# Kernel tuning notes

Measured on AMD Instinct MI355X. Metric: run time of the kernel, lower is better.

The kernel has to match this reference:

```python
import jax, jax.numpy as jnp
import numpy as np

B, T, TEMP_IN, STAT_IN = 8, 512, 32, 16
TEMP_H, STAT_H, ATTN_H, N_LAYERS, N_CLS = 64, 32, 32, 2, 2
BN_INV = float(1.0 / np.sqrt(1.0 + 1e-5))  # eval-mode BN, running_mean=0, running_var=1


def _bn(x, g, b):
    return x * (g * BN_INV) + b


def _lrelu(x):
    return jax.nn.leaky_relu(x, 0.01)


def _mlp_layer(x, W, b, g, beta):
    return _lrelu(_bn(x @ W + b, g, beta))


def setup_inputs() -> dict:
    key = jax.random.key(0)
    ks = jax.random.split(key, 32)
    lengths = jax.random.randint(ks[0], (B,), T // 2, T + 1)
    mask_q = jnp.arange(T)[None, :] < lengths[:, None]          # [B,T]
    masks = mask_q[:, :, None]                                   # [B,T,1] bool
    x_temp = jax.random.normal(ks[1], (B, T, TEMP_IN), jnp.float32) * mask_q[..., None]
    x_stat = jax.random.normal(ks[2], (B, STAT_IN), jnp.float32)
    t = jnp.sort(jax.random.uniform(ks[3], (B, T), jnp.float32) * 100.0, axis=-1)
    p = lambda k, sh, s=0.1: jax.random.normal(k, sh, jnp.float32) * s
    inp = dict(x_temp=x_temp, x_stat=x_stat, t=t, masks=masks, lengths=lengths)
    # attn_mlp: Linear(1,H)+BN+LeakyReLU, Linear(H,1)
    inp['aw0'] = p(ks[4], (1, ATTN_H), 0.5); inp['ab0'] = p(ks[5], (ATTN_H,))
    inp['ag'] = 1.0 + p(ks[6], (ATTN_H,)); inp['abeta'] = p(ks[7], (ATTN_H,))
    inp['aw1'] = p(ks[8], (ATTN_H, 1), 0.2); inp['ab1'] = p(ks[9], (1,))
    # top non_linear_temp / non_linear_stat
    inp['tw'] = p(ks[10], (TEMP_IN, TEMP_H)); inp['tb'] = p(ks[11], (TEMP_H,))
    inp['tg'] = 1.0 + p(ks[12], (TEMP_H,)); inp['tbeta'] = p(ks[13], (TEMP_H,))
    inp['sw'] = p(ks[14], (STAT_IN, STAT_H)); inp['sb'] = p(ks[15], (STAT_H,))
    inp['sg'] = 1.0 + p(ks[16], (STAT_H,)); inp['sbeta'] = p(ks[17], (STAT_H,))
    # stacked SimtaPlusLayer params [L,...]
    inp['lw_t'] = p(ks[18], (N_LAYERS, TEMP_H + STAT_H, TEMP_H))
    inp['lb_t'] = p(ks[19], (N_LAYERS, TEMP_H))
    inp['lg_t'] = 1.0 + p(ks[20], (N_LAYERS, TEMP_H)); inp['lbeta_t'] = p(ks[21], (N_LAYERS, TEMP_H))
    inp['lw_s'] = p(ks[22], (N_LAYERS, STAT_H, STAT_H))
    inp['lb_s'] = p(ks[23], (N_LAYERS, STAT_H))
    inp['lg_s'] = 1.0 + p(ks[24], (N_LAYERS, STAT_H)); inp['lbeta_s'] = p(ks[25], (N_LAYERS, STAT_H))
    inp['cw'] = p(ks[26], (TEMP_H + STAT_H, N_CLS)); inp['cb'] = p(ks[27], (N_CLS,))
    return inp


def _forward(x_temp, x_stat, t, aw0, ab0, ag, abeta, aw1, ab1, tw, tb, tg, tbeta,
             sw, sb, sg, sbeta, lw_t, lb_t, lg_t, lbeta_t, lw_s, lb_s, lg_s, lbeta_s,
             cw, cb, mask_q):
    # dt[b,i,j] = (t[b,j]-t[b,i]) / (max dt + eps)
    dt = t[:, None, :] - t[:, :, None]
    dt = dt / (dt.max() + 1e-8)
    # pairwise-MLP temporal attention: [B,T,T,H] intermediate (memory-bound)
    h = _lrelu(_bn(dt[..., None] * aw0[0] + ab0, ag, abeta))
    a = (h @ aw1)[..., 0] + ab1[0]                                # [B,T,T]
    temp_attn = jax.nn.softmax(jnp.where(mask_q[:, None, :], a, -9e8), axis=-1)

    x_t = _mlp_layer(x_temp, tw, tb, tg, tbeta)                   # [B,T,Ct]
    x_s = _mlp_layer(x_stat, sw, sb, sg, sbeta)                   # [B,Cs]

    for l in range(lw_t.shape[0]):
        xs_rep = jnp.broadcast_to(x_s[:, None, :], (x_t.shape[0], x_t.shape[1], x_s.shape[-1]))
        x = _mlp_layer(jnp.concatenate([x_t, xs_rep], axis=-1), lw_t[l], lb_t[l], lg_t[l], lbeta_t[l])
        x = x * mask_q[..., None]                                 # pad_packed zeros invalid rows
        d = jnp.asarray(x.shape[-1], x.dtype)
        qk = jnp.einsum('bic,bjc->bij', x, x) / jnp.sqrt(d)
        self_attn = jax.nn.softmax(qk, axis=-1)                   # torch softmaxes over all keys (pads give qk=0)
        attn = (self_attn + temp_attn) * mask_q[:, None, :]       # masked_fill(~mask, 0) on key columns
        x_s = _mlp_layer(x_s, lw_s[l], lb_s[l], lg_s[l], lbeta_s[l])
        x_t = (attn @ x) * mask_q[..., None]

    xs_rep = jnp.broadcast_to(x_s[:, None, :], (x_t.shape[0], x_t.shape[1], x_s.shape[-1]))
    output = jnp.concatenate([x_t, xs_rep], axis=-1) @ cw + cb    # [B,T,C]
    output = output * mask_q[..., None]
    # per-segment argmax over (logit1 - logit0), gather that row
    diff = jnp.where(mask_q, output[..., 1] - output[..., 0], -1e30)
    idx = jnp.argmax(diff, axis=1)                                # [B]
    output_max = output[jnp.arange(output.shape[0]), idx]         # [B,C]
    return output, output_max


def reference(x_temp, x_stat, t, masks, lengths, aw0, ab0, ag, abeta, aw1, ab1,
              tw, tb, tg, tbeta, sw, sb, sg, sbeta,
              lw_t, lb_t, lg_t, lbeta_t, lw_s, lb_s, lg_s, lbeta_s, cw, cb):
    mask_q = jnp.any(masks, axis=-1)                              # [B,T]
    return _forward(x_temp, x_stat, t, aw0, ab0, ag, abeta, aw1, ab1, tw, tb, tg, tbeta,
                    sw, sb, sg, sbeta, lw_t, lb_t, lg_t, lbeta_t, lw_s, lb_s, lg_s, lbeta_s,
                    cw, cb, mask_q)
```

## Files before the change

### kernel.cpp

```cpp
#include <hip/hip_runtime.h>

#define B 8
#define T 512
#define TEMP_IN 32
#define STAT_IN 16
#define TEMP_H 64
#define STAT_H 32
#define ATTN_H 32
#define N_CLS 2
#define BN_INV 0.99999500003749969f
#define R 8

struct KP {
    const float *x_temp, *x_stat, *t;
    const int* lengths;
    const float *aw0, *ab0, *ag, *abeta, *aw1, *ab1;
    const float *tw, *tb, *tg, *tbeta;
    const float *sw, *sb, *sg, *sbeta;
    const float *lw_t, *lb_t, *lg_t, *lbeta_t;
    const float *lw_s, *lb_s, *lg_s, *lbeta_s;
    const float *cw, *cb;
    float *XL, *XL2;
    unsigned long long* cand;
    unsigned *f1, *f2;
    unsigned *arr;
    float *out, *outmax;
};

__device__ __forceinline__ float lrelu(float x) {
    return fmaxf(x, 0.01f * x);
}
__device__ __forceinline__ float wave_max(float x) {
    #pragma unroll
    for (int o = 32; o > 0; o >>= 1) x = fmaxf(x, __shfl_xor(x, o));
    return x;
}
__device__ __forceinline__ float wave_sum(float x) {
    #pragma unroll
    for (int o = 32; o > 0; o >>= 1) x += __shfl_xor(x, o);
    return x;
}
__device__ __forceinline__ unsigned ordf(float f) {
    unsigned u = __float_as_uint(f);
    return (u & 0x80000000u) ? ~u : (u | 0x80000000u);
}

__device__ __forceinline__ void stg_llc(float* p, float v) {
    __hip_atomic_store(p, v, __ATOMIC_RELAXED, __HIP_MEMORY_SCOPE_AGENT);
}
__device__ __forceinline__ float ldg_llc(const float* p) {
    return __hip_atomic_load(p, __ATOMIC_RELAXED, __HIP_MEMORY_SCOPE_AGENT);
}
__device__ __forceinline__ void drain_vm() {
    asm volatile("s_waitcnt vmcnt(0)" ::: "memory");
}
__device__ __forceinline__ void fence_acq_wg() {
    __builtin_amdgcn_fence(__ATOMIC_ACQUIRE, "workgroup");
}

struct Shm {
    float att[R][T];
    float part[4][R][TEMP_H];
    float xi[R][TEMP_H];
    float x1[R][TEMP_H];
    float t_s[T];
    float s_w[3 * ATTN_H + 1];
    float xs[3][STAT_H];
    float xr[4][TEMP_IN];
    float h0s[4][TEMP_H + STAT_H];
    float o_rc[R][2];
    int lastf;
};

__device__ __forceinline__ void publish(unsigned* f) {
    drain_vm();
    __syncthreads();
    if (threadIdx.x == 0)
        __hip_atomic_store(f, 1u, __ATOMIC_RELAXED, __HIP_MEMORY_SCOPE_AGENT);
}
__device__ __forceinline__ void wait_batch(const unsigned* fbase, int tid) {
    if (tid < 64) {
        const unsigned* p = fbase + tid * 16;
        while (__hip_atomic_load(p, __ATOMIC_RELAXED, __HIP_MEMORY_SCOPE_AGENT) == 0u)
            __builtin_amdgcn_s_sleep(4);
    }
    __syncthreads();
    fence_acq_wg();
}

__device__ __forceinline__ void front(const KP& P, Shm& S, int b, int i0, int len,
                                      int lane, int wave) {
    #pragma unroll
    for (int p = 0; p < 2; ++p) {
        int r = p * 4 + wave;
        int i = i0 + r;
        int row = b * T + i;
        if (lane < TEMP_IN) S.xr[wave][lane] = P.x_temp[row * TEMP_IN + lane];
        __syncthreads();
        float acc = P.tb[lane];
        #pragma unroll
        for (int k = 0; k < TEMP_IN; ++k) acc += S.xr[wave][k] * P.tw[k * TEMP_H + lane];
        acc = acc * (P.tg[lane] * BN_INV) + P.tbeta[lane];
        S.h0s[wave][lane] = lrelu(acc);
        if (lane < STAT_H) S.h0s[wave][TEMP_H + lane] = S.xs[0][lane];
        __syncthreads();
        float a2 = P.lb_t[lane];
        #pragma unroll
        for (int k = 0; k < TEMP_H + STAT_H; ++k) a2 += S.h0s[wave][k] * P.lw_t[k * TEMP_H + lane];
        a2 = a2 * (P.lg_t[lane] * BN_INV) + P.lbeta_t[lane];
        a2 = lrelu(a2);
        stg_llc(&P.XL[(size_t)row * TEMP_H + lane], (i < len) ? a2 : 0.f);
        __syncthreads();
    }
}

__device__ __forceinline__ void temp_compute(Shm& S, float tmpv[2][8], float inv_dt,
                                             int i0, int len, int lane, int wave) {
    float ab1v = S.s_w[3 * ATTN_H];
    #pragma unroll
    for (int rr = 0; rr < 2; ++rr) {
        int r = wave + rr * 4;
        float ti = S.t_s[i0 + r];
        float a[8], dtq[8];
        #pragma unroll
        for (int q = 0; q < 8; ++q) {
            dtq[q] = (S.t_s[lane + q * 64] - ti) * inv_dt;
            a[q] = ab1v;
        }
        #pragma unroll 4
        for (int k = 0; k < ATTN_H; ++k) {
            float Wk = S.s_w[k];
            float Ck = S.s_w[ATTN_H + k];
            float w1k = S.s_w[2 * ATTN_H + k];
            #pragma unroll
            for (int q = 0; q < 8; ++q) {
                float h = dtq[q] * Wk + Ck;
                h = fmaxf(h, 0.01f * h);
                a[q] += h * w1k;
            }
        }
        float m2 = -1e30f;
        #pragma unroll
        for (int q = 0; q < 8; ++q) {
            int j = lane + q * 64;
            a[q] = (j < len) ? a[q] : -9e8f;
            m2 = fmaxf(m2, a[q]);
        }
        m2 = wave_max(m2);
        float s2 = 0.f;
        #pragma unroll
        for (int q = 0; q < 8; ++q) { a[q] = __expf(a[q] - m2); s2 += a[q]; }
        s2 = wave_sum(s2);
        float inv2 = 1.0f / s2;
        #pragma unroll
        for (int q = 0; q < 8; ++q) tmpv[rr][q] = a[q] * inv2;
    }
}

template <int EPI, bool LOAD_XI>
__device__ __forceinline__ void attn_core(const KP& P, Shm& S, const float* src,
                                          const float tmpv[2][8],
                                          int b, int i0, int len, int tid, int lane, int wave,
                                          int tile) {
    if (LOAD_XI) {
        for (int idx = tid; idx < R * TEMP_H; idx += 256)
            S.xi[idx >> 6][idx & 63] = src[((size_t)(b * T + i0 + (idx >> 6))) * TEMP_H + (idx & 63)];
    }
    __syncthreads();
    for (int j = tid; j < T; j += 256) {
        const float4* xj4 = reinterpret_cast<const float4*>(&src[((size_t)(b * T + j)) * TEMP_H]);
        float acc[R];
        #pragma unroll
        for (int r = 0; r < R; ++r) acc[r] = 0.f;
        #pragma unroll
        for (int c4 = 0; c4 < TEMP_H / 4; ++c4) {
            float4 xv = xj4[c4];
            #pragma unroll
            for (int r = 0; r < R; ++r) {
                float4 xi4 = *reinterpret_cast<const float4*>(&S.xi[r][c4 * 4]);
                acc[r] += xi4.x * xv.x + xi4.y * xv.y + xi4.z * xv.z + xi4.w * xv.w;
            }
        }
        #pragma unroll
        for (int r = 0; r < R; ++r) S.att[r][j] = acc[r] * 0.125f;
    }
    __syncthreads();
    #pragma unroll
    for (int rr = 0; rr < 2; ++rr) {
        int r = wave + rr * 4;
        float v[8];
        float m = -1e30f;
        #pragma unroll
        for (int q = 0; q < 8; ++q) { v[q] = S.att[r][lane + q * 64]; m = fmaxf(m, v[q]); }
        m = wave_max(m);
        float s = 0.f;
        #pragma unroll
        for (int q = 0; q < 8; ++q) { v[q] = __expf(v[q] - m); s += v[q]; }
        s = wave_sum(s);
        float invs = 1.0f / s;
        #pragma unroll
        for (int q = 0; q < 8; ++q) {
            int j = lane + q * 64;
            S.att[r][j] = (j < len) ? (v[q] * invs + tmpv[rr][q]) : 0.f;
        }
    }
    __syncthreads();
    float acc2[R];
    #pragma unroll
    for (int r = 0; r < R; ++r) acc2[r] = 0.f;
    {
        const float* srow = src + (size_t)b * T * TEMP_H + lane;
        int j0 = wave * 128;
        for (int g = 0; g < 32; ++g) {
            int j = j0 + g * 4;
            float xv0 = srow[(size_t)(j + 0) * TEMP_H];
            float xv1 = srow[(size_t)(j + 1) * TEMP_H];
            float xv2 = srow[(size_t)(j + 2) * TEMP_H];
            float xv3 = srow[(size_t)(j + 3) * TEMP_H];
            #pragma unroll
            for (int r = 0; r < R; ++r) {
                float4 a4 = *reinterpret_cast<const float4*>(&S.att[r][j]);
                acc2[r] += a4.x * xv0 + a4.y * xv1 + a4.z * xv2 + a4.w * xv3;
            }
        }
    }
    #pragma unroll
    for (int r = 0; r < R; ++r) S.part[wave][r][lane] = acc2[r];
    __syncthreads();
    for (int idx = tid; idx < R * TEMP_H; idx += 256) {
        int r = idx >> 6, cc = idx & 63;
        float sum = S.part[0][r][cc] + S.part[1][r][cc] + S.part[2][r][cc] + S.part[3][r][cc];
        S.x1[r][cc] = ((i0 + r) < len) ? sum : 0.f;
    }
    __syncthreads();

    if (EPI == 0) {
        const float* lw1    = P.lw_t + (TEMP_H + STAT_H) * TEMP_H;
        const float* lb1    = P.lb_t + TEMP_H;
        const float* lg1    = P.lg_t + TEMP_H;
        const float* lbeta1 = P.lbeta_t + TEMP_H;
        #pragma unroll
        for (int rr = 0; rr < 2; ++rr) {
            int r = wave * 2 + rr;
            int i = i0 + r;
            float acc = lb1[lane];
            #pragma unroll
            for (int k = 0; k < TEMP_H; ++k) acc += S.x1[r][k] * lw1[k * TEMP_H + lane];
            #pragma unroll
            for (int k = 0; k < STAT_H; ++k) acc += S.xs[1][k] * lw1[(TEMP_H + k) * TEMP_H + lane];
            acc = acc * (lg1[lane] * BN_INV) + lbeta1[lane];
            acc = lrelu(acc);
            float vout = (i < len) ? acc : 0.f;
            stg_llc(&P.XL2[((size_t)(b * T + i)) * TEMP_H + lane], vout);
            S.xi[r][lane] = vout;
        }
    } else {
        if (tid < R * N_CLS) {
            int r = tid >> 1, cls = tid & 1;
            int i = i0 + r;
            float o = P.cb[cls];
            #pragma unroll
            for (int k = 0; k < TEMP_H; ++k) o += S.x1[r][k] * P.cw[k * N_CLS + cls];
            #pragma unroll
            for (int k = 0; k < STAT_H; ++k) o += S.xs[2][k] * P.cw[(TEMP_H + k) * N_CLS + cls];
            if (i >= len) o = 0.f;
            stg_llc(&P.out[((size_t)(b * T + i)) * N_CLS + cls], o);
            S.o_rc[r][cls] = o;
        }
        __syncthreads();
        if (tid == 0) {
            float best = -3e30f; int bi = i0;
            for (int r = 0; r < R; ++r) {
                int i = i0 + r;
                float diff = (i < len) ? (S.o_rc[r][1] - S.o_rc[r][0]) : -1e30f;
                if (diff > best) { best = diff; bi = i; }
            }
            unsigned long long pack =
                ((unsigned long long)ordf(best) << 32) | (unsigned)(~(unsigned)bi);
            __hip_atomic_store(&P.cand[(b * 64 + tile) * 8], pack,
                               __ATOMIC_RELAXED, __HIP_MEMORY_SCOPE_AGENT);
            drain_vm();
            unsigned old = __hip_atomic_fetch_add(&P.arr[b * 16], 1u,
                                                  __ATOMIC_RELAXED, __HIP_MEMORY_SCOPE_AGENT);
            S.lastf = (old == 63u) ? 1 : 0;
        }
        __syncthreads();
        if (S.lastf) {
            fence_acq_wg();
            if (tid < 64) {
                unsigned long long c = __hip_atomic_load(&P.cand[(b * 64 + tid) * 8],
                                                         __ATOMIC_RELAXED, __HIP_MEMORY_SCOPE_AGENT);
                #pragma unroll
                for (int o = 32; o > 0; o >>= 1) {
                    unsigned long long oc = __shfl_xor(c, o);
                    c = (oc > c) ? oc : c;
                }
                if (tid == 0) {
                    int idx = (int)(~(unsigned)(c & 0xffffffffu));
                    float o0 = ldg_llc(&P.out[((size_t)(b * T + idx)) * N_CLS + 0]);
                    float o1 = ldg_llc(&P.out[((size_t)(b * T + idx)) * N_CLS + 1]);
                    stg_llc(&P.outmax[b * 2 + 0], o0);
                    stg_llc(&P.outmax[b * 2 + 1], o1);
                }
            }
        }
    }
}

template <int PHASE>
__global__ void __launch_bounds__(256, 2) k_run(KP P) {
    __shared__ Shm S;
    int tid = threadIdx.x, lane = tid & 63, wave = tid >> 6;
    int blk = blockIdx.x;
    int b = blk & 7, tile = blk >> 3, i0 = tile * R;
    int len = P.lengths[b];
    float tmpv[2][8];

    if (tid < STAT_H) {
        float acc = P.sb[tid];
        #pragma unroll
        for (int k = 0; k < STAT_IN; ++k) acc += P.x_stat[b * STAT_IN + k] * P.sw[k * STAT_H + tid];
        acc = acc * (P.sg[tid] * BN_INV) + P.sbeta[tid];
        S.xs[0][tid] = lrelu(acc);
    }
    __syncthreads();

    if (PHASE == 0 || PHASE == 3) front(P, S, b, i0, len, lane, wave);
    if (PHASE == 3) publish(&P.f1[(b * 64 + tile) * 16]);

    if (PHASE != 0) {
        if (tid < ATTN_H) {
            float g = P.ag[tid] * BN_INV;
            S.s_w[tid]              = P.aw0[tid] * g;
            S.s_w[ATTN_H + tid]     = P.ab0[tid] * g + P.abeta[tid];
            S.s_w[2 * ATTN_H + tid] = P.aw1[tid];
        }
        if (tid == 0) S.s_w[3 * ATTN_H] = P.ab1[0];
        S.t_s[tid] = P.t[b * T + tid];
        S.t_s[tid + 256] = P.t[b * T + tid + 256];
        float d = P.t[(lane & 7) * T + (T - 1)] - P.t[(lane & 7) * T];
        d = wave_max(d);
        float inv_dt = 1.0f / (d + 1e-8f);
        __syncthreads();
        if (tid < STAT_H) {
            float a2 = P.lb_s[tid];
            #pragma unroll
            for (int k = 0; k < STAT_H; ++k) a2 += S.xs[0][k] * P.lw_s[k * STAT_H + tid];
            a2 = a2 * (P.lg_s[tid] * BN_INV) + P.lbeta_s[tid];
            S.xs[1][tid] = lrelu(a2);
        }
        __syncthreads();
        if (tid < STAT_H) {
            float a2 = P.lb_s[STAT_H + tid];
            #pragma unroll
            for (int k = 0; k < STAT_H; ++k) a2 += S.xs[1][k] * P.lw_s[(STAT_H + k) * STAT_H + tid];
            a2 = a2 * (P.lg_s[STAT_H + tid] * BN_INV) + P.lbeta_s[STAT_H + tid];
            S.xs[2][tid] = lrelu(a2);
        }
        __syncthreads();
        temp_compute(S, tmpv, inv_dt, i0, len, lane, wave);
        __syncthreads();
    }

    if (PHASE == 3) wait_batch(P.f1 + b * 64 * 16, tid);
    if (PHASE == 1 || PHASE == 3)
        attn_core<0, true>(P, S, P.XL, tmpv, b, i0, len, tid, lane, wave, tile);
    if (PHASE == 3) {
        publish(&P.f2[(b * 64 + tile) * 16]);
        wait_batch(P.f2 + b * 64 * 16, tid);
        attn_core<1, false>(P, S, P.XL2, tmpv, b, i0, len, tid, lane, wave, tile);
    } else if (PHASE == 2) {
        attn_core<1, true>(P, S, P.XL2, tmpv, b, i0, len, tid, lane, wave, tile);
    }
}

extern "C" void kernel_launch(void* const* d_in, const int* in_sizes, int n_in,
                              void* d_out, int out_size, void* d_ws, size_t ws_size,
                              hipStream_t stream) {
    KP p;
    p.x_temp  = (const float*)d_in[0];
    p.x_stat  = (const float*)d_in[1];
    p.t       = (const float*)d_in[2];
    p.lengths = (const int*)d_in[4];
    p.aw0 = (const float*)d_in[5];
    p.ab0 = (const float*)d_in[6];
    p.ag  = (const float*)d_in[7];
    p.abeta = (const float*)d_in[8];
    p.aw1 = (const float*)d_in[9];
    p.ab1 = (const float*)d_in[10];
    p.tw  = (const float*)d_in[11];
    p.tb  = (const float*)d_in[12];
    p.tg  = (const float*)d_in[13];
    p.tbeta = (const float*)d_in[14];
    p.sw  = (const float*)d_in[15];
    p.sb  = (const float*)d_in[16];
    p.sg  = (const float*)d_in[17];
    p.sbeta = (const float*)d_in[18];
    p.lw_t = (const float*)d_in[19];
    p.lb_t = (const float*)d_in[20];
    p.lg_t = (const float*)d_in[21];
    p.lbeta_t = (const float*)d_in[22];
    p.lw_s = (const float*)d_in[23];
    p.lb_s = (const float*)d_in[24];
    p.lg_s = (const float*)d_in[25];
    p.lbeta_s = (const float*)d_in[26];
    p.cw = (const float*)d_in[27];
    p.cb = (const float*)d_in[28];

    float* ws = (float*)d_ws;
    p.XL  = ws;
    p.XL2 = ws + (size_t)B * T * TEMP_H;
    p.cand = (unsigned long long*)(ws + 2 * (size_t)B * T * TEMP_H);
    p.f1  = (unsigned*)(p.cand + B * 64 * 8);
    p.f2  = p.f1 + B * 64 * 16;
    p.arr = p.f2 + B * 64 * 16;
    p.out = (float*)d_out;
    p.outmax = p.out + (size_t)B * T * N_CLS;

    size_t flagbytes = (size_t)B * 64 * 8 * 8 + 2 * (size_t)B * 64 * 16 * 4 + (size_t)B * 16 * 4;
    hipMemsetAsync(p.cand, 0, flagbytes, stream);

    void* args[] = { (void*)&p };
    hipError_t err = hipLaunchCooperativeKernel((const void*)k_run<3>, dim3(B * (T / R)),
                                                dim3(256), args, 0, stream);
    if (err != hipSuccess) {
        (void)hipGetLastError();
        k_run<0><<<B * (T / R), 256, 0, stream>>>(p);
        k_run<1><<<B * (T / R), 256, 0, stream>>>(p);
        k_run<2><<<B * (T / R), 256, 0, stream>>>(p);
    }
}
```

Before: 103.4 us.

## Merge two row tiles into 512-thread blocks, halving grid and sync flags

Each block now runs 512 threads split into two 256-thread sides, each handling 8 query rows, so the grid shrinks from 512 to 256 blocks covering 16 rows apiece. Each batch now waits on 32 per-block flags instead of 64, which cuts grid-barrier polling, and the shared per-batch setup (time vector, stat MLP) is done once for 16 rows. Front-stage scratch now shares shared memory with the partial-sum buffer through a union. The cost is larger blocks with more shared memory and possibly lower occupancy per CU, and the grid may now fill fewer CUs.

```diff
diff --git a/kernel.cpp b/kernel.cpp
--- a/kernel.cpp
+++ b/kernel.cpp
@@ -9,7 +9,8 @@
 #define ATTN_H 32
 #define N_CLS 2
 #define BN_INV 0.99999500003749969f
-#define R 8
+#define NBLK 256
+#define NT2  32
 
 struct KP {
     const float *x_temp, *x_stat, *t;
@@ -44,7 +45,6 @@
     unsigned u = __float_as_uint(f);
     return (u & 0x80000000u) ? ~u : (u | 0x80000000u);
 }
-
 __device__ __forceinline__ void stg_llc(float* p, float v) {
     __hip_atomic_store(p, v, __ATOMIC_RELAXED, __HIP_MEMORY_SCOPE_AGENT);
 }
@@ -59,16 +59,17 @@
 }
 
 struct Shm {
-    float att[R][T];
-    float part[4][R][TEMP_H];
-    float xi[R][TEMP_H];
-    float x1[R][TEMP_H];
+    float att[2][8][T];
+    union {
+        float part[2][4][8][TEMP_H];
+        struct { float xr[8][TEMP_IN]; float h0s[8][TEMP_H + STAT_H]; } fr;
+    } u;
+    float xi[2][8][TEMP_H];
+    float x1[2][8][TEMP_H];
     float t_s[T];
     float s_w[3 * ATTN_H + 1];
     float xs[3][STAT_H];
-    float xr[4][TEMP_IN];
-    float h0s[4][TEMP_H + STAT_H];
-    float o_rc[R][2];
+    float o_rc[16][2];
     int lastf;
 };
 
@@ -79,7 +80,7 @@
         __hip_atomic_store(f, 1u, __ATOMIC_RELAXED, __HIP_MEMORY_SCOPE_AGENT);
 }
 __device__ __forceinline__ void wait_batch(const unsigned* fbase, int tid) {
-    if (tid < 64) {
+    if (tid < NT2) {
         const unsigned* p = fbase + tid * 16;
         while (__hip_atomic_load(p, __ATOMIC_RELAXED, __HIP_MEMORY_SCOPE_AGENT) == 0u)
             __builtin_amdgcn_s_sleep(4);
@@ -88,25 +89,25 @@
     fence_acq_wg();
 }
 
-__device__ __forceinline__ void front(const KP& P, Shm& S, int b, int i0, int len,
+__device__ __forceinline__ void front(const KP& P, Shm& S, int b, int i0b, int len,
                                       int lane, int wave) {
     #pragma unroll
     for (int p = 0; p < 2; ++p) {
-        int r = p * 4 + wave;
-        int i = i0 + r;
+        int r = p * 8 + wave;
+        int i = i0b + r;
         int row = b * T + i;
-        if (lane < TEMP_IN) S.xr[wave][lane] = P.x_temp[row * TEMP_IN + lane];
+        if (lane < TEMP_IN) S.u.fr.xr[wave][lane] = P.x_temp[row * TEMP_IN + lane];
         __syncthreads();
         float acc = P.tb[lane];
         #pragma unroll
-        for (int k = 0; k < TEMP_IN; ++k) acc += S.xr[wave][k] * P.tw[k * TEMP_H + lane];
+        for (int k = 0; k < TEMP_IN; ++k) acc += S.u.fr.xr[wave][k] * P.tw[k * TEMP_H + lane];
         acc = acc * (P.tg[lane] * BN_INV) + P.tbeta[lane];
-        S.h0s[wave][lane] = lrelu(acc);
-        if (lane < STAT_H) S.h0s[wave][TEMP_H + lane] = S.xs[0][lane];
+        S.u.fr.h0s[wave][lane] = lrelu(acc);
+        if (lane < STAT_H) S.u.fr.h0s[wave][TEMP_H + lane] = S.xs[0][lane];
         __syncthreads();
         float a2 = P.lb_t[lane];
         #pragma unroll
-        for (int k = 0; k < TEMP_H + STAT_H; ++k) a2 += S.h0s[wave][k] * P.lw_t[k * TEMP_H + lane];
+        for (int k = 0; k < TEMP_H + STAT_H; ++k) a2 += S.u.fr.h0s[wave][k] * P.lw_t[k * TEMP_H + lane];
         a2 = a2 * (P.lg_t[lane] * BN_INV) + P.lbeta_t[lane];
         a2 = lrelu(a2);
         stg_llc(&P.XL[(size_t)row * TEMP_H + lane], (i < len) ? a2 : 0.f);
@@ -115,12 +116,12 @@
 }
 
 __device__ __forceinline__ void temp_compute(Shm& S, float tmpv[2][8], float inv_dt,
-                                             int i0, int len, int lane, int wave) {
+                                             int i0s, int len, int lane, int swave) {
     float ab1v = S.s_w[3 * ATTN_H];
     #pragma unroll
     for (int rr = 0; rr < 2; ++rr) {
-        int r = wave + rr * 4;
-        float ti = S.t_s[i0 + r];
+        int r = swave + rr * 4;
+        float ti = S.t_s[i0s + r];
         float a[8], dtq[8];
         #pragma unroll
         for (int q = 0; q < 8; ++q) {
@@ -160,38 +161,41 @@
 template <int EPI, bool LOAD_XI>
 __device__ __forceinline__ void attn_core(const KP& P, Shm& S, const float* src,
                                           const float tmpv[2][8],
-                                          int b, int i0, int len, int tid, int lane, int wave,
-                                          int tile) {
+                                          int b, int i0b, int len,
+                                          int tid, int lane, int side, int stid, int swave,
+                                          int blk_id) {
+    int i0s = i0b + side * 8;
     if (LOAD_XI) {
-        for (int idx = tid; idx < R * TEMP_H; idx += 256)
-            S.xi[idx >> 6][idx & 63] = src[((size_t)(b * T + i0 + (idx >> 6))) * TEMP_H + (idx & 63)];
-    }
-    __syncthreads();
-    for (int j = tid; j < T; j += 256) {
+        for (int idx = stid; idx < 8 * TEMP_H; idx += 256)
+            S.xi[side][idx >> 6][idx & 63] =
+                src[((size_t)(b * T + i0s + (idx >> 6))) * TEMP_H + (idx & 63)];
+    }
+    __syncthreads();
+    for (int j = stid; j < T; j += 256) {
         const float4* xj4 = reinterpret_cast<const float4*>(&src[((size_t)(b * T + j)) * TEMP_H]);
-        float acc[R];
-        #pragma unroll
-        for (int r = 0; r < R; ++r) acc[r] = 0.f;
+        float acc[8];
+        #pragma unroll
+        for (int r = 0; r < 8; ++r) acc[r] = 0.f;
         #pragma unroll
         for (int c4 = 0; c4 < TEMP_H / 4; ++c4) {
             float4 xv = xj4[c4];
             #pragma unroll
-            for (int r = 0; r < R; ++r) {
-                float4 xi4 = *reinterpret_cast<const float4*>(&S.xi[r][c4 * 4]);
+            for (int r = 0; r < 8; ++r) {
+                float4 xi4 = *reinterpret_cast<const float4*>(&S.xi[side][r][c4 * 4]);
                 acc[r] += xi4.x * xv.x + xi4.y * xv.y + xi4.z * xv.z + xi4.w * xv.w;
             }
         }
         #pragma unroll
-        for (int r = 0; r < R; ++r) S.att[r][j] = acc[r] * 0.125f;
+        for (int r = 0; r < 8; ++r) S.att[side][r][j] = acc[r] * 0.125f;
     }
     __syncthreads();
     #pragma unroll
     for (int rr = 0; rr < 2; ++rr) {
-        int r = wave + rr * 4;
+        int r = swave + rr * 4;
         float v[8];
         float m = -1e30f;
         #pragma unroll
-        for (int q = 0; q < 8; ++q) { v[q] = S.att[r][lane + q * 64]; m = fmaxf(m, v[q]); }
+        for (int q = 0; q < 8; ++q) { v[q] = S.att[side][r][lane + q * 64]; m = fmaxf(m, v[q]); }
         m = wave_max(m);
         float s = 0.f;
         #pragma unroll
@@ -201,16 +205,16 @@
         #pragma unroll
         for (int q = 0; q < 8; ++q) {
             int j = lane + q * 64;
-            S.att[r][j] = (j < len) ? (v[q] * invs + tmpv[rr][q]) : 0.f;
-        }
-    }
-    __syncthreads();
-    float acc2[R];
-    #pragma unroll
-    for (int r = 0; r < R; ++r) acc2[r] = 0.f;
+            S.att[side][r][j] = (j < len) ? (v[q] * invs + tmpv[rr][q]) : 0.f;
+        }
+    }
+    __syncthreads();
+    float acc2[8];
+    #pragma unroll
+    for (int r = 0; r < 8; ++r) acc2[r] = 0.f;
     {
         const float* srow = src + (size_t)b * T * TEMP_H + lane;
-        int j0 = wave * 128;
+        int j0 = swave * 128;
         for (int g = 0; g < 32; ++g) {
             int j = j0 + g * 4;
             float xv0 = srow[(size_t)(j + 0) * TEMP_H];
@@ -218,19 +222,20 @@
             float xv2 = srow[(size_t)(j + 2) * TEMP_H];
             float xv3 = srow[(size_t)(j + 3) * TEMP_H];
             #pragma unroll
-            for (int r = 0; r < R; ++r) {
-                float4 a4 = *reinterpret_cast<const float4*>(&S.att[r][j]);
+            for (int r = 0; r < 8; ++r) {
+                float4 a4 = *reinterpret_cast<const float4*>(&S.att[side][r][j]);
                 acc2[r] += a4.x * xv0 + a4.y * xv1 + a4.z * xv2 + a4.w * xv3;
             }
         }
     }
     #pragma unroll
-    for (int r = 0; r < R; ++r) S.part[wave][r][lane] = acc2[r];
-    __syncthreads();
-    for (int idx = tid; idx < R * TEMP_H; idx += 256) {
+    for (int r = 0; r < 8; ++r) S.u.part[side][swave][r][lane] = acc2[r];
+    __syncthreads();
+    for (int idx = stid; idx < 8 * TEMP_H; idx += 256) {
         int r = idx >> 6, cc = idx & 63;
-        float sum = S.part[0][r][cc] + S.part[1][r][cc] + S.part[2][r][cc] + S.part[3][r][cc];
-        S.x1[r][cc] = ((i0 + r) < len) ? sum : 0.f;
+        float sum = S.u.part[side][0][r][cc] + S.u.part[side][1][r][cc]
+                  + S.u.part[side][2][r][cc] + S.u.part[side][3][r][cc];
+        S.x1[side][r][cc] = ((i0s + r) < len) ? sum : 0.f;
     }
     __syncthreads();
 
@@ -241,57 +246,57 @@
         const float* lbeta1 = P.lbeta_t + TEMP_H;
         #pragma unroll
         for (int rr = 0; rr < 2; ++rr) {
-            int r = wave * 2 + rr;
-            int i = i0 + r;
+            int r = swave * 2 + rr;
+            int i = i0s + r;
             float acc = lb1[lane];
             #pragma unroll
-            for (int k = 0; k < TEMP_H; ++k) acc += S.x1[r][k] * lw1[k * TEMP_H + lane];
+            for (int k = 0; k < TEMP_H; ++k) acc += S.x1[side][r][k] * lw1[k * TEMP_H + lane];
             #pragma unroll
             for (int k = 0; k < STAT_H; ++k) acc += S.xs[1][k] * lw1[(TEMP_H + k) * TEMP_H + lane];
             acc = acc * (lg1[lane] * BN_INV) + lbeta1[lane];
             acc = lrelu(acc);
             float vout = (i < len) ? acc : 0.f;
             stg_llc(&P.XL2[((size_t)(b * T + i)) * TEMP_H + lane], vout);
-            S.xi[r][lane] = vout;
+            S.xi[side][r][lane] = vout;
         }
     } else {
-        if (tid < R * N_CLS) {
-            int r = tid >> 1, cls = tid & 1;
-            int i = i0 + r;
+        if (stid < 8 * N_CLS) {
+            int r = stid >> 1, cls = stid & 1;
+            int i = i0s + r;
             float o = P.cb[cls];
             #pragma unroll
-            for (int k = 0; k < TEMP_H; ++k) o += S.x1[r][k] * P.cw[k * N_CLS + cls];
+            for (int k = 0; k < TEMP_H; ++k) o += S.x1[side][r][k] * P.cw[k * N_CLS + cls];
             #pragma unroll
             for (int k = 0; k < STAT_H; ++k) o += S.xs[2][k] * P.cw[(TEMP_H + k) * N_CLS + cls];
             if (i >= len) o = 0.f;
             stg_llc(&P.out[((size_t)(b * T + i)) * N_CLS + cls], o);
-            S.o_rc[r][cls] = o;
+            S.o_rc[side * 8 + r][cls] = o;
         }
         __syncthreads();
         if (tid == 0) {
-            float best = -3e30f; int bi = i0;
-            for (int r = 0; r < R; ++r) {
-                int i = i0 + r;
+            float best = -3e30f; int bi = i0b;
+            for (int r = 0; r < 16; ++r) {
+                int i = i0b + r;
                 float diff = (i < len) ? (S.o_rc[r][1] - S.o_rc[r][0]) : -1e30f;
                 if (diff > best) { best = diff; bi = i; }
             }
             unsigned long long pack =
                 ((unsigned long long)ordf(best) << 32) | (unsigned)(~(unsigned)bi);
-            __hip_atomic_store(&P.cand[(b * 64 + tile) * 8], pack,
+            __hip_atomic_store(&P.cand[blk_id * 8], pack,
                                __ATOMIC_RELAXED, __HIP_MEMORY_SCOPE_AGENT);
             drain_vm();
             unsigned old = __hip_atomic_fetch_add(&P.arr[b * 16], 1u,
                                                   __ATOMIC_RELAXED, __HIP_MEMORY_SCOPE_AGENT);
-            S.lastf = (old == 63u) ? 1 : 0;
+            S.lastf = (old == (NT2 - 1)) ? 1 : 0;
         }
         __syncthreads();
         if (S.lastf) {
             fence_acq_wg();
-            if (tid < 64) {
-                unsigned long long c = __hip_atomic_load(&P.cand[(b * 64 + tid) * 8],
+            if (tid < NT2) {
+                unsigned long long c = __hip_atomic_load(&P.cand[(b * NT2 + tid) * 8],
                                                          __ATOMIC_RELAXED, __HIP_MEMORY_SCOPE_AGENT);
                 #pragma unroll
-                for (int o = 32; o > 0; o >>= 1) {
+                for (int o = 16; o > 0; o >>= 1) {
                     unsigned long long oc = __shfl_xor(c, o);
                     c = (oc > c) ? oc : c;
                 }
@@ -308,11 +313,16 @@
 }
 
 template <int PHASE>
-__global__ void __launch_bounds__(256, 2) k_run(KP P) {
+__global__ void __launch_bounds__(512) k_run(KP P) {
     __shared__ Shm S;
-    int tid = threadIdx.x, lane = tid & 63, wave = tid >> 6;
+    int tid = threadIdx.x;
+    int lane = tid & 63, wave = tid >> 6;
+    int side = wave >> 2, swave = wave & 3;
+    int stid = tid & 255;
     int blk = blockIdx.x;
-    int b = blk & 7, tile = blk >> 3, i0 = tile * R;
+    int b = blk & 7, t2 = blk >> 3;
+    int blk_id = b * NT2 + t2;
+    int i0b = t2 * 16;
     int len = P.lengths[b];
     float tmpv[2][8];
 
@@ -325,8 +335,8 @@
     }
     __syncthreads();
 
-    if (PHASE == 0 || PHASE == 3) front(P, S, b, i0, len, lane, wave);
-    if (PHASE == 3) publish(&P.f1[(b * 64 + tile) * 16]);
+    if (PHASE == 0 || PHASE == 3) front(P, S, b, i0b, len, lane, wave);
+    if (PHASE == 3) publish(&P.f1[blk_id * 16]);
 
     if (PHASE != 0) {
         if (tid < ATTN_H) {
@@ -337,7 +347,6 @@
         }
         if (tid == 0) S.s_w[3 * ATTN_H] = P.ab1[0];
         S.t_s[tid] = P.t[b * T + tid];
-        S.t_s[tid + 256] = P.t[b * T + tid + 256];
         float d = P.t[(lane & 7) * T + (T - 1)] - P.t[(lane & 7) * T];
         d = wave_max(d);
         float inv_dt = 1.0f / (d + 1e-8f);
@@ -358,19 +367,19 @@
             S.xs[2][tid] = lrelu(a2);
         }
         __syncthreads();
-        temp_compute(S, tmpv, inv_dt, i0, len, lane, wave);
-        __syncthreads();
-    }
-
-    if (PHASE == 3) wait_batch(P.f1 + b * 64 * 16, tid);
+        temp_compute(S, tmpv, inv_dt, i0b + side * 8, len, lane, swave);
+        __syncthreads();
+    }
+
+    if (PHASE == 3) wait_batch(P.f1 + b * NT2 * 16, tid);
     if (PHASE == 1 || PHASE == 3)
-        attn_core<0, true>(P, S, P.XL, tmpv, b, i0, len, tid, lane, wave, tile);
+        attn_core<0, true>(P, S, P.XL, tmpv, b, i0b, len, tid, lane, side, stid, swave, blk_id);
     if (PHASE == 3) {
-        publish(&P.f2[(b * 64 + tile) * 16]);
-        wait_batch(P.f2 + b * 64 * 16, tid);
-        attn_core<1, false>(P, S, P.XL2, tmpv, b, i0, len, tid, lane, wave, tile);
+        publish(&P.f2[blk_id * 16]);
+        wait_batch(P.f2 + b * NT2 * 16, tid);
+        attn_core<1, false>(P, S, P.XL2, tmpv, b, i0b, len, tid, lane, side, stid, swave, blk_id);
     } else if (PHASE == 2) {
-        attn_core<1, true>(P, S, P.XL2, tmpv, b, i0, len, tid, lane, wave, tile);
+        attn_core<1, true>(P, S, P.XL2, tmpv, b, i0b, len, tid, lane, side, stid, swave, blk_id);
     }
 }
 
@@ -411,22 +420,22 @@
     p.XL  = ws;
     p.XL2 = ws + (size_t)B * T * TEMP_H;
     p.cand = (unsigned long long*)(ws + 2 * (size_t)B * T * TEMP_H);
-    p.f1  = (unsigned*)(p.cand + B * 64 * 8);
-    p.f2  = p.f1 + B * 64 * 16;
-    p.arr = p.f2 + B * 64 * 16;
+    p.f1  = (unsigned*)(p.cand + B * NT2 * 8);
+    p.f2  = p.f1 + B * NT2 * 16;
+    p.arr = p.f2 + B * NT2 * 16;
     p.out = (float*)d_out;
     p.outmax = p.out + (size_t)B * T * N_CLS;
 
-    size_t flagbytes = (size_t)B * 64 * 8 * 8 + 2 * (size_t)B * 64 * 16 * 4 + (size_t)B * 16 * 4;
+    size_t flagbytes = (size_t)B * NT2 * 8 * 8 + 2 * (size_t)B * NT2 * 16 * 4 + (size_t)B * 16 * 4;
     hipMemsetAsync(p.cand, 0, flagbytes, stream);
 
     void* args[] = { (void*)&p };
-    hipError_t err = hipLaunchCooperativeKernel((const void*)k_run<3>, dim3(B * (T / R)),
-                                                dim3(256), args, 0, stream);
+    hipError_t err = hipLaunchCooperativeKernel((const void*)k_run<3>, dim3(NBLK),
+                                                dim3(512), args, 0, stream);
     if (err != hipSuccess) {
         (void)hipGetLastError();
-        k_run<0><<<B * (T / R), 256, 0, stream>>>(p);
-        k_run<1><<<B * (T / R), 256, 0, stream>>>(p);
-        k_run<2><<<B * (T / R), 256, 0, stream>>>(p);
-    }
-}
+        k_run<0><<<NBLK, 512, 0, stream>>>(p);
+        k_run<1><<<NBLK, 512, 0, stream>>>(p);
+        k_run<2><<<NBLK, 512, 0, stream>>>(p);
+    }
+}
```

New measurement: 104.5 us. Within noise of the previous version (+1.1%).

## Halve rows per block to four and double the cooperative grid

Applied to the files above, without the earlier changes.

Each block now handles 4 query rows instead of 8, so the grid doubles to 1024 blocks and launch bounds allow 4 blocks per CU. Per-row loops collapse to one row per wave, flag waits and candidate reduction cover 128 tiles per batch, and workspace sizing follows NTILE. This aims for more parallelism and shorter per-block latency. In exchange, each block re-reads the full key/value matrix for half as many rows, doubling that traffic, and the cooperative launch needs all 1024 blocks resident at once.

```diff
diff --git a/kernel.cpp b/kernel.cpp
--- a/kernel.cpp
+++ b/kernel.cpp
@@ -9,7 +9,8 @@
 #define ATTN_H 32
 #define N_CLS 2
 #define BN_INV 0.99999500003749969f
-#define R 8
+#define R 4
+#define NTILE (T / R)
 
 struct KP {
     const float *x_temp, *x_stat, *t;
@@ -44,7 +45,6 @@
     unsigned u = __float_as_uint(f);
     return (u & 0x80000000u) ? ~u : (u | 0x80000000u);
 }
-
 __device__ __forceinline__ void stg_llc(float* p, float v) {
     __hip_atomic_store(p, v, __ATOMIC_RELAXED, __HIP_MEMORY_SCOPE_AGENT);
 }
@@ -79,7 +79,7 @@
         __hip_atomic_store(f, 1u, __ATOMIC_RELAXED, __HIP_MEMORY_SCOPE_AGENT);
 }
 __device__ __forceinline__ void wait_batch(const unsigned* fbase, int tid) {
-    if (tid < 64) {
+    if (tid < NTILE) {
         const unsigned* p = fbase + tid * 16;
         while (__hip_atomic_load(p, __ATOMIC_RELAXED, __HIP_MEMORY_SCOPE_AGENT) == 0u)
             __builtin_amdgcn_s_sleep(4);
@@ -90,81 +90,73 @@
 
 __device__ __forceinline__ void front(const KP& P, Shm& S, int b, int i0, int len,
                                       int lane, int wave) {
-    #pragma unroll
-    for (int p = 0; p < 2; ++p) {
-        int r = p * 4 + wave;
-        int i = i0 + r;
-        int row = b * T + i;
-        if (lane < TEMP_IN) S.xr[wave][lane] = P.x_temp[row * TEMP_IN + lane];
-        __syncthreads();
-        float acc = P.tb[lane];
-        #pragma unroll
-        for (int k = 0; k < TEMP_IN; ++k) acc += S.xr[wave][k] * P.tw[k * TEMP_H + lane];
-        acc = acc * (P.tg[lane] * BN_INV) + P.tbeta[lane];
-        S.h0s[wave][lane] = lrelu(acc);
-        if (lane < STAT_H) S.h0s[wave][TEMP_H + lane] = S.xs[0][lane];
-        __syncthreads();
-        float a2 = P.lb_t[lane];
-        #pragma unroll
-        for (int k = 0; k < TEMP_H + STAT_H; ++k) a2 += S.h0s[wave][k] * P.lw_t[k * TEMP_H + lane];
-        a2 = a2 * (P.lg_t[lane] * BN_INV) + P.lbeta_t[lane];
-        a2 = lrelu(a2);
-        stg_llc(&P.XL[(size_t)row * TEMP_H + lane], (i < len) ? a2 : 0.f);
-        __syncthreads();
-    }
-}
-
-__device__ __forceinline__ void temp_compute(Shm& S, float tmpv[2][8], float inv_dt,
+    int i = i0 + wave;
+    int row = b * T + i;
+    if (lane < TEMP_IN) S.xr[wave][lane] = P.x_temp[row * TEMP_IN + lane];
+    __syncthreads();
+    float acc = P.tb[lane];
+    #pragma unroll
+    for (int k = 0; k < TEMP_IN; ++k) acc += S.xr[wave][k] * P.tw[k * TEMP_H + lane];
+    acc = acc * (P.tg[lane] * BN_INV) + P.tbeta[lane];
+    S.h0s[wave][lane] = lrelu(acc);
+    if (lane < STAT_H) S.h0s[wave][TEMP_H + lane] = S.xs[0][lane];
+    __syncthreads();
+    float a2 = P.lb_t[lane];
+    #pragma unroll
+    for (int k = 0; k < TEMP_H + STAT_H; ++k) a2 += S.h0s[wave][k] * P.lw_t[k * TEMP_H + lane];
+    a2 = a2 * (P.lg_t[lane] * BN_INV) + P.lbeta_t[lane];
+    a2 = lrelu(a2);
+    stg_llc(&P.XL[(size_t)row * TEMP_H + lane], (i < len) ? a2 : 0.f);
+    __syncthreads();
+}
+
+__device__ __forceinline__ void temp_compute(Shm& S, float tmpv[8], float inv_dt,
                                              int i0, int len, int lane, int wave) {
     float ab1v = S.s_w[3 * ATTN_H];
-    #pragma unroll
-    for (int rr = 0; rr < 2; ++rr) {
-        int r = wave + rr * 4;
-        float ti = S.t_s[i0 + r];
-        float a[8], dtq[8];
+    float ti = S.t_s[i0 + wave];
+    float a[8], dtq[8];
+    #pragma unroll
+    for (int q = 0; q < 8; ++q) {
+        dtq[q] = (S.t_s[lane + q * 64] - ti) * inv_dt;
+        a[q] = ab1v;
+    }
+    #pragma unroll 4
+    for (int k = 0; k < ATTN_H; ++k) {
+        float Wk = S.s_w[k];
+        float Ck = S.s_w[ATTN_H + k];
+        float w1k = S.s_w[2 * ATTN_H + k];
         #pragma unroll
         for (int q = 0; q < 8; ++q) {
-            dtq[q] = (S.t_s[lane + q * 64] - ti) * inv_dt;
-            a[q] = ab1v;
-        }
-        #pragma unroll 4
-        for (int k = 0; k < ATTN_H; ++k) {
-            float Wk = S.s_w[k];
-            float Ck = S.s_w[ATTN_H + k];
-            float w1k = S.s_w[2 * ATTN_H + k];
-            #pragma unroll
-            for (int q = 0; q < 8; ++q) {
-                float h = dtq[q] * Wk + Ck;
-                h = fmaxf(h, 0.01f * h);
-                a[q] += h * w1k;
-            }
-        }
-        float m2 = -1e30f;
-        #pragma unroll
-        for (int q = 0; q < 8; ++q) {
-            int j = lane + q * 64;
-            a[q] = (j < len) ? a[q] : -9e8f;
-            m2 = fmaxf(m2, a[q]);
-        }
-        m2 = wave_max(m2);
-        float s2 = 0.f;
-        #pragma unroll
-        for (int q = 0; q < 8; ++q) { a[q] = __expf(a[q] - m2); s2 += a[q]; }
-        s2 = wave_sum(s2);
-        float inv2 = 1.0f / s2;
-        #pragma unroll
-        for (int q = 0; q < 8; ++q) tmpv[rr][q] = a[q] * inv2;
-    }
+            float h = dtq[q] * Wk + Ck;
+            h = fmaxf(h, 0.01f * h);
+            a[q] += h * w1k;
+        }
+    }
+    float m2 = -1e30f;
+    #pragma unroll
+    for (int q = 0; q < 8; ++q) {
+        int j = lane + q * 64;
+        a[q] = (j < len) ? a[q] : -9e8f;
+        m2 = fmaxf(m2, a[q]);
+    }
+    m2 = wave_max(m2);
+    float s2 = 0.f;
+    #pragma unroll
+    for (int q = 0; q < 8; ++q) { a[q] = __expf(a[q] - m2); s2 += a[q]; }
+    s2 = wave_sum(s2);
+    float inv2 = 1.0f / s2;
+    #pragma unroll
+    for (int q = 0; q < 8; ++q) tmpv[q] = a[q] * inv2;
 }
 
 template <int EPI, bool LOAD_XI>
 __device__ __forceinline__ void attn_core(const KP& P, Shm& S, const float* src,
-                                          const float tmpv[2][8],
+                                          const float tmpv[8],
                                           int b, int i0, int len, int tid, int lane, int wave,
-                                          int tile) {
+                                          int blk_id) {
     if (LOAD_XI) {
-        for (int idx = tid; idx < R * TEMP_H; idx += 256)
-            S.xi[idx >> 6][idx & 63] = src[((size_t)(b * T + i0 + (idx >> 6))) * TEMP_H + (idx & 63)];
+        if (tid < R * TEMP_H)
+            S.xi[tid >> 6][tid & 63] = src[((size_t)(b * T + i0 + (tid >> 6))) * TEMP_H + (tid & 63)];
     }
     __syncthreads();
     for (int j = tid; j < T; j += 256) {
@@ -185,9 +177,8 @@
         for (int r = 0; r < R; ++r) S.att[r][j] = acc[r] * 0.125f;
     }
     __syncthreads();
-    #pragma unroll
-    for (int rr = 0; rr < 2; ++rr) {
-        int r = wave + rr * 4;
+    {
+        int r = wave;
         float v[8];
         float m = -1e30f;
         #pragma unroll
@@ -201,7 +192,7 @@
         #pragma unroll
         for (int q = 0; q < 8; ++q) {
             int j = lane + q * 64;
-            S.att[r][j] = (j < len) ? (v[q] * invs + tmpv[rr][q]) : 0.f;
+            S.att[r][j] = (j < len) ? (v[q] * invs + tmpv[q]) : 0.f;
         }
     }
     __syncthreads();
@@ -227,8 +218,8 @@
     #pragma unroll
     for (int r = 0; r < R; ++r) S.part[wave][r][lane] = acc2[r];
     __syncthreads();
-    for (int idx = tid; idx < R * TEMP_H; idx += 256) {
-        int r = idx >> 6, cc = idx & 63;
+    {
+        int r = wave, cc = lane;
         float sum = S.part[0][r][cc] + S.part[1][r][cc] + S.part[2][r][cc] + S.part[3][r][cc];
         S.x1[r][cc] = ((i0 + r) < len) ? sum : 0.f;
     }
@@ -239,21 +230,19 @@
         const float* lb1    = P.lb_t + TEMP_H;
         const float* lg1    = P.lg_t + TEMP_H;
         const float* lbeta1 = P.lbeta_t + TEMP_H;
-        #pragma unroll
-        for (int rr = 0; rr < 2; ++rr) {
-            int r = wave * 2 + rr;
-            int i = i0 + r;
-            float acc = lb1[lane];
-            #pragma unroll
-            for (int k = 0; k < TEMP_H; ++k) acc += S.x1[r][k] * lw1[k * TEMP_H + lane];
-            #pragma unroll
-            for (int k = 0; k < STAT_H; ++k) acc += S.xs[1][k] * lw1[(TEMP_H + k) * TEMP_H + lane];
-            acc = acc * (lg1[lane] * BN_INV) + lbeta1[lane];
-            acc = lrelu(acc);
-            float vout = (i < len) ? acc : 0.f;
-            stg_llc(&P.XL2[((size_t)(b * T + i)) * TEMP_H + lane], vout);
-            S.xi[r][lane] = vout;
-        }
+        int r = wave;
+        int i = i0 + r;
+        float acc = lb1[lane];
+        #pragma unroll
+        for (int k = 0; k < TEMP_H; ++k) acc += S.x1[r][k] * lw1[k * TEMP_H + lane];
+        #pragma unroll
+        for (int k = 0; k < STAT_H; ++k) acc += S.xs[1][k] * lw1[(TEMP_H + k) * TEMP_H + lane];
+        acc = acc * (lg1[lane] * BN_INV) + lbeta1[lane];
+        acc = lrelu(acc);
+        float vout = (i < len) ? acc : 0.f;
+        stg_llc(&P.XL2[((size_t)(b * T + i)) * TEMP_H + lane], vout);
+        __syncthreads();
+        S.xi[r][lane] = vout;
     } else {
         if (tid < R * N_CLS) {
             int r = tid >> 1, cls = tid & 1;
@@ -277,19 +266,22 @@
             }
             unsigned long long pack =
                 ((unsigned long long)ordf(best) << 32) | (unsigned)(~(unsigned)bi);
-            __hip_atomic_store(&P.cand[(b * 64 + tile) * 8], pack,
+            __hip_atomic_store(&P.cand[blk_id * 8], pack,
                                __ATOMIC_RELAXED, __HIP_MEMORY_SCOPE_AGENT);
             drain_vm();
             unsigned old = __hip_atomic_fetch_add(&P.arr[b * 16], 1u,
                                                   __ATOMIC_RELAXED, __HIP_MEMORY_SCOPE_AGENT);
-            S.lastf = (old == 63u) ? 1 : 0;
+            S.lastf = (old == (NTILE - 1)) ? 1 : 0;
         }
         __syncthreads();
         if (S.lastf) {
             fence_acq_wg();
             if (tid < 64) {
-                unsigned long long c = __hip_atomic_load(&P.cand[(b * 64 + tid) * 8],
-                                                         __ATOMIC_RELAXED, __HIP_MEMORY_SCOPE_AGENT);
+                unsigned long long c0 = __hip_atomic_load(&P.cand[(b * NTILE + tid) * 8],
+                                                          __ATOMIC_RELAXED, __HIP_MEMORY_SCOPE_AGENT);
+                unsigned long long c1 = __hip_atomic_load(&P.cand[(b * NTILE + 64 + tid) * 8],
+                                                          __ATOMIC_RELAXED, __HIP_MEMORY_SCOPE_AGENT);
+                unsigned long long c = (c1 > c0) ? c1 : c0;
                 #pragma unroll
                 for (int o = 32; o > 0; o >>= 1) {
                     unsigned long long oc = __shfl_xor(c, o);
@@ -308,13 +300,14 @@
 }
 
 template <int PHASE>
-__global__ void __launch_bounds__(256, 2) k_run(KP P) {
+__global__ void __launch_bounds__(256, 4) k_run(KP P) {
     __shared__ Shm S;
     int tid = threadIdx.x, lane = tid & 63, wave = tid >> 6;
     int blk = blockIdx.x;
     int b = blk & 7, tile = blk >> 3, i0 = tile * R;
+    int blk_id = b * NTILE + tile;
     int len = P.lengths[b];
-    float tmpv[2][8];
+    float tmpv[8];
 
     if (tid < STAT_H) {
         float acc = P.sb[tid];
@@ -326,7 +319,7 @@
     __syncthreads();
 
     if (PHASE == 0 || PHASE == 3) front(P, S, b, i0, len, lane, wave);
-    if (PHASE == 3) publish(&P.f1[(b * 64 + tile) * 16]);
+    if (PHASE == 3) publish(&P.f1[blk_id * 16]);
 
     if (PHASE != 0) {
         if (tid < ATTN_H) {
@@ -362,15 +355,15 @@
         __syncthreads();
     }
 
-    if (PHASE == 3) wait_batch(P.f1 + b * 64 * 16, tid);
+    if (PHASE == 3) wait_batch(P.f1 + b * NTILE * 16, tid);
     if (PHASE == 1 || PHASE == 3)
-        attn_core<0, true>(P, S, P.XL, tmpv, b, i0, len, tid, lane, wave, tile);
+        attn_core<0, true>(P, S, P.XL, tmpv, b, i0, len, tid, lane, wave, blk_id);
     if (PHASE == 3) {
-        publish(&P.f2[(b * 64 + tile) * 16]);
-        wait_batch(P.f2 + b * 64 * 16, tid);
-        attn_core<1, false>(P, S, P.XL2, tmpv, b, i0, len, tid, lane, wave, tile);
+        publish(&P.f2[blk_id * 16]);
+        wait_batch(P.f2 + b * NTILE * 16, tid);
+        attn_core<1, false>(P, S, P.XL2, tmpv, b, i0, len, tid, lane, wave, blk_id);
     } else if (PHASE == 2) {
-        attn_core<1, true>(P, S, P.XL2, tmpv, b, i0, len, tid, lane, wave, tile);
+        attn_core<1, true>(P, S, P.XL2, tmpv, b, i0, len, tid, lane, wave, blk_id);
     }
 }
 
@@ -411,22 +404,23 @@
     p.XL  = ws;
     p.XL2 = ws + (size_t)B * T * TEMP_H;
     p.cand = (unsigned long long*)(ws + 2 * (size_t)B * T * TEMP_H);
-    p.f1  = (unsigned*)(p.cand + B * 64 * 8);
-    p.f2  = p.f1 + B * 64 * 16;
-    p.arr = p.f2 + B * 64 * 16;
+    p.f1  = (unsigned*)(p.cand + B * NTILE * 8);
+    p.f2  = p.f1 + B * NTILE * 16;
+    p.arr = p.f2 + B * NTILE * 16;
     p.out = (float*)d_out;
     p.outmax = p.out + (size_t)B * T * N_CLS;
 
-    size_t flagbytes = (size_t)B * 64 * 8 * 8 + 2 * (size_t)B * 64 * 16 * 4 + (size_t)B * 16 * 4;
+    size_t flagbytes = (size_t)B * NTILE * 8 * 8
+                     + 2 * (size_t)B * NTILE * 16 * 4 + (size_t)B * 16 * 4;
     hipMemsetAsync(p.cand, 0, flagbytes, stream);
 
     void* args[] = { (void*)&p };
-    hipError_t err = hipLaunchCooperativeKernel((const void*)k_run<3>, dim3(B * (T / R)),
+    hipError_t err = hipLaunchCooperativeKernel((const void*)k_run<3>, dim3(B * NTILE),
                                                 dim3(256), args, 0, stream);
     if (err != hipSuccess) {
         (void)hipGetLastError();
-        k_run<0><<<B * (T / R), 256, 0, stream>>>(p);
-        k_run<1><<<B * (T / R), 256, 0, stream>>>(p);
-        k_run<2><<<B * (T / R), 256, 0, stream>>>(p);
-    }
-}
+        k_run<0><<<B * NTILE, 256, 0, stream>>>(p);
+        k_run<1><<<B * NTILE, 256, 0, stream>>>(p);
+        k_run<2><<<B * NTILE, 256, 0, stream>>>(p);
+    }
+}
```

Result: faster. 101.1 us (median of 2 runs) (-2.2%).
